# Optimization experiments

Measured on AMD Instinct MI355X. Metric: run time of the kernel, lower is better.

Reference implementation:

```python
import jax, jax.numpy as jnp
import numpy as np

# Mamba2 hyperparameters (from init_kwargs + mamba_ssm defaults)
D_MODEL = 1024
D_STATE = 64
D_CONV = 4
EXPAND = 2
HEADDIM = 64                      # mamba_ssm default
D_INNER = EXPAND * D_MODEL        # 2048
NHEADS = D_INNER // HEADDIM       # 32
NGROUPS = 1
CONV_DIM = D_INNER + 2 * NGROUPS * D_STATE      # 2176
D_IN_PROJ = 2 * D_INNER + 2 * NGROUPS * D_STATE + NHEADS  # 4256
BATCH, SEQLEN = 4, 2048


def setup_inputs() -> dict:
    key = jax.random.key(0)
    ks = jax.random.split(key, 8)
    x = jax.random.normal(ks[0], (BATCH, SEQLEN, D_MODEL), dtype=jnp.float32)
    W_in = jax.random.normal(ks[1], (D_MODEL, D_IN_PROJ), dtype=jnp.float32) * 0.02
    conv_w = jax.random.normal(ks[2], (CONV_DIM, D_CONV), dtype=jnp.float32) * 0.2
    conv_b = jnp.zeros((CONV_DIM,), dtype=jnp.float32)
    # dt_bias = inverse-softplus of dt ~ U(1e-3, 0.1), as in mamba_ssm init
    dt = jnp.exp(jax.random.uniform(ks[3], (NHEADS,)) * (np.log(0.1) - np.log(1e-3)) + np.log(1e-3))
    dt_bias = dt + jnp.log(-jnp.expm1(-dt))
    A_log = jnp.log(jax.random.uniform(ks[4], (NHEADS,), minval=1.0, maxval=16.0))
    D = jnp.ones((NHEADS,), dtype=jnp.float32)
    norm_w = jnp.ones((D_INNER,), dtype=jnp.float32)
    W_out = jax.random.normal(ks[5], (D_INNER, D_MODEL), dtype=jnp.float32) * 0.02
    return {"x": x, "W_in": W_in, "conv_w": conv_w, "conv_b": conv_b,
            "dt_bias": dt_bias, "A_log": A_log, "D": D, "norm_w": norm_w, "W_out": W_out}


def _mamba2_forward(x, W_in, conv_w, conv_b, dt_bias, A_log, D, norm_w, W_out):
    Bsz, L, _ = x.shape
    zxbcdt = x @ W_in                                   # [B, L, D_IN_PROJ]
    z = zxbcdt[..., :D_INNER]                           # gate
    xBC = zxbcdt[..., D_INNER:D_INNER + CONV_DIM]
    dt = zxbcdt[..., D_INNER + CONV_DIM:]               # [B, L, H]
    dt = jax.nn.softplus(dt + dt_bias)

    # causal depthwise conv1d over time, kernel width D_CONV
    xp = jnp.pad(xBC, ((0, 0), (D_CONV - 1, 0), (0, 0)))
    xc = sum(xp[:, k:k + L, :] * conv_w[:, k] for k in range(D_CONV))
    xBC = jax.nn.silu(xc + conv_b)

    xh = xBC[..., :D_INNER].reshape(Bsz, L, NHEADS, HEADDIM)   # [B,L,H,P]
    Bm = xBC[..., D_INNER:D_INNER + D_STATE]                   # [B,L,N] (ngroups=1)
    Cm = xBC[..., D_INNER + D_STATE:]                          # [B,L,N]
    A = -jnp.exp(A_log)                                        # [H]

    # selective SSM scan: h_t = h_{t-1}*exp(dt_t*A) + dt_t * x_t (outer) B_t ; y_t = C_t . h_t
    def step(h, inp):
        dt_t, x_t, B_t, C_t = inp                 # [B,H],[B,H,P],[B,N],[B,N]
        dA = jnp.exp(dt_t * A)                    # [B,H]
        h = h * dA[..., None, None] + (dt_t[..., None] * x_t)[..., None] * B_t[:, None, None, :]
        y_t = jnp.einsum('bhpn,bn->bhp', h, C_t)
        return h, y_t

    h0 = jnp.zeros((Bsz, NHEADS, HEADDIM, D_STATE), dtype=x.dtype)
    inputs = (jnp.moveaxis(dt, 1, 0), jnp.moveaxis(xh, 1, 0),
              jnp.moveaxis(Bm, 1, 0), jnp.moveaxis(Cm, 1, 0))
    _, ys = jax.lax.scan(step, h0, inputs)                     # [L,B,H,P]
    y = jnp.moveaxis(ys, 0, 1) + xh * D[None, None, :, None]   # skip term D*x
    y = y.reshape(Bsz, L, D_INNER)

    # gated RMSNorm: norm(y * silu(z)) * weight
    y = y * jax.nn.silu(z)
    y = y * jax.lax.rsqrt(jnp.mean(y * y, axis=-1, keepdims=True) + 1e-5) * norm_w
    return y @ W_out


def reference(x, W_in, conv_w, conv_b, dt_bias, A_log, D, norm_w, W_out):
    return _mamba2_forward(x, W_in, conv_w, conv_b, dt_bias, A_log, D, norm_w, W_out)
```

## Files before the change

### kernel.cpp

```cpp
#include <hip/hip_runtime.h>
#include <hip/hip_bf16.h>

#define B_SZ   4
#define SEQ    2048
#define DM     1024
#define DIN    2048
#define DST    64
#define NH     32
#define HD     64
#define CONVD  2176
#define DPROJ  4256
#define NPROJ  4224
#define MROWS  (B_SZ*SEQ)
#define QC     64
#define NC     (SEQ/QC)


typedef __attribute__((ext_vector_type(8))) __bf16 bf16x8;
typedef __attribute__((ext_vector_type(4))) __bf16 bf16x4;
typedef __attribute__((ext_vector_type(4))) float  floatx4;

__device__ __forceinline__ int swz(int row, int col) {
    return row * 64 + ((((col >> 3) ^ (row & 7)) << 3) | (col & 7));
}
__device__ __forceinline__ float bfbits2f(unsigned short u) {
    return __uint_as_float(((unsigned int)u) << 16);
}
__device__ __forceinline__ unsigned short f2bfbits(float f) {
    union { __bf16 h; unsigned short u; } cv; cv.h = (__bf16)f; return cv.u;
}

__global__ __launch_bounds__(256) void prep_weights_kernel(const float* __restrict__ W_in,
                                                           const float* __restrict__ W_out,
                                                           const float* __restrict__ norm_w,
                                                           float* __restrict__ dtWc,
                                                           __bf16* __restrict__ WinT,
                                                           __bf16* __restrict__ WoutT) {
    __shared__ float tile[32][129];
    const int bid = blockIdx.x, tid = threadIdx.x;
    if (bid < 128) {
        int idx = bid * 256 + tid;
        int k = idx >> 5, h = idx & 31;
        dtWc[idx] = W_in[(size_t)k * DPROJ + 2 * DIN + 2 * DST + h];
        return;
    }
    const float* src; __bf16* dst; const float* scal; int Ksrc, Csrc, mb, kb;
    if (bid < 128 + 1056) {
        int t = bid - 128; mb = t >> 5; kb = t & 31;
        src = W_in; dst = WinT; scal = nullptr; Ksrc = DM; Csrc = DPROJ;
    } else {
        int t = bid - 1184; mb = t >> 6; kb = t & 63;
        src = W_out; dst = WoutT; scal = norm_w; Ksrc = DIN; Csrc = DM;
    }
    const int K32 = Ksrc >> 5;
    #pragma unroll
    for (int i = 0; i < 4; i++) {
        int idx = tid + 256 * i;
        int kl = idx >> 5, c4 = idx & 31;
        int n = mb * 128 + c4 * 4;
        float4 v = make_float4(0.f, 0.f, 0.f, 0.f);
        if (n < Csrc) v = *(const float4*)(src + (size_t)(kb * 32 + kl) * Csrc + n);
        if (scal) { float s = scal[kb * 32 + kl]; v.x *= s; v.y *= s; v.z *= s; v.w *= s; }
        tile[kl][c4 * 4 + 0] = v.x; tile[kl][c4 * 4 + 1] = v.y;
        tile[kl][c4 * 4 + 2] = v.z; tile[kl][c4 * 4 + 3] = v.w;
    }
    __syncthreads();
    #pragma unroll
    for (int i = 0; i < 2; i++) {
        int c = tid + 256 * i;
        int sub = c >> 6, ln = c & 63, q = ln >> 4, lmn = ln & 15;
        bf16x8 o;
        #pragma unroll
        for (int e = 0; e < 8; e++) o[e] = (__bf16)tile[q * 8 + e][sub * 16 + lmn];
        *(bf16x8*)(dst + ((((size_t)(mb * 8 + sub)) * K32 + kb) << 9) + (ln << 3)) = o;
    }
}

__global__ __launch_bounds__(256) void cvt_dt_kernel(const float* __restrict__ x,
                                                     const float* __restrict__ dtWc,
                                                     __bf16* __restrict__ xbf,
                                                     float* __restrict__ dtraw) {
    __shared__ float xs[16][132];
    __shared__ float dtw[128 * 32];
    const int tid = threadIdx.x;
    const int r0 = blockIdx.x * 16;
    const int lm = tid & 15, pos = tid >> 4;
    const int rr = tid >> 4, h2 = (tid & 15) * 2;
    __bf16* slab = xbf + (size_t)blockIdx.x * (16 * DM);

    float a0 = 0.f, a1 = 0.f;
    for (int kc = 0; kc < 8; kc++) {
        #pragma unroll
        for (int i = 0; i < 2; i++) {
            int idx = tid + 256 * i;
            int row = idx >> 5, c4 = idx & 31;
            float4 v = ((const float4*)(x + (size_t)(r0 + row) * DM + kc * 128))[c4];
            xs[row][c4 * 4 + 0] = v.x; xs[row][c4 * 4 + 1] = v.y;
            xs[row][c4 * 4 + 2] = v.z; xs[row][c4 * 4 + 3] = v.w;
        }
        #pragma unroll
        for (int i = 0; i < 16; i++)
            dtw[tid + 256 * i] = dtWc[kc * 4096 + tid + 256 * i];
        __syncthreads();
        {
            bf16x8 o;
            #pragma unroll
            for (int e = 0; e < 8; e++) o[e] = (__bf16)xs[lm][pos * 8 + e];
            int kb = kc * 4 + (pos >> 2), q = pos & 3;
            *(bf16x8*)(slab + (size_t)(kb * 64 + q * 16 + lm) * 8) = o;
        }
        for (int j = 0; j < 128; j++) {
            float xv = xs[rr][j];
            a0 = fmaf(xv, dtw[j * 32 + h2], a0);
            a1 = fmaf(xv, dtw[j * 32 + h2 + 1], a1);
        }
        __syncthreads();
    }
    dtraw[(size_t)(r0 + rr) * NH + h2]     = a0;
    dtraw[(size_t)(r0 + rr) * NH + h2 + 1] = a1;
}

template<int STORE_BF16>
__global__ __launch_bounds__(256) void gemm_tt_kernel(const __bf16* __restrict__ A,
                                                      const __bf16* __restrict__ Bt,
                                                      float* __restrict__ Cf,
                                                      __bf16* __restrict__ Cb,
                                                      const float* __restrict__ rowscale,
                                                      int N, int K) {
    __shared__ __align__(16) __bf16 As[4096];
    __shared__ __align__(16) __bf16 Bs[4096];
    const int tid = threadIdx.x;
    const int wave = tid >> 6, lane = tid & 63;
    const int lm = lane & 15, lq = lane >> 4;
    const int mb = blockIdx.x, nb = blockIdx.y;
    const int K32 = K >> 5;

    floatx4 acc[4][4] = {};

    for (int kb = 0; kb < K32; kb++) {
        #pragma unroll
        for (int r = 0; r < 2; r++) {
            int c = tid + (r << 8);
            int sub = c >> 6, ln = c & 63;
            __builtin_amdgcn_global_load_lds(
                reinterpret_cast<const unsigned int*>(
                    A + ((((size_t)(mb * 8 + sub)) * K32 + kb) << 9) + (ln << 3)),
                reinterpret_cast<unsigned int*>(As + (size_t)c * 8), 16, 0, 0);
            __builtin_amdgcn_global_load_lds(
                reinterpret_cast<const unsigned int*>(
                    Bt + ((((size_t)(nb * 8 + sub)) * K32 + kb) << 9) + (ln << 3)),
                reinterpret_cast<unsigned int*>(Bs + (size_t)c * 8), 16, 0, 0);
        }
        __syncthreads();
        bf16x8 af[4], bfr[4];
        #pragma unroll
        for (int i = 0; i < 4; i++)
            af[i] = *(const bf16x8*)(As + ((((wave & 1) << 2) + i) << 9) + (lane << 3));
        #pragma unroll
        for (int i = 0; i < 4; i++)
            bfr[i] = *(const bf16x8*)(Bs + ((((wave >> 1) << 2) + i) << 9) + (lane << 3));
        #pragma unroll
        for (int mi = 0; mi < 4; mi++)
            #pragma unroll
            for (int ni = 0; ni < 4; ni++)
                acc[mi][ni] = __builtin_amdgcn_mfma_f32_16x16x32_bf16(af[mi], bfr[ni], acc[mi][ni], 0, 0, 0);
        __syncthreads();
    }

    const int wm = (wave & 1) << 6, wn = (wave >> 1) << 6;
    #pragma unroll
    for (int mi = 0; mi < 4; mi++) {
        #pragma unroll
        for (int r = 0; r < 4; r++) {
            int row = mb * 128 + wm + mi * 16 + lq * 4 + r;
            float s = 1.f;
            if (rowscale) s = rsqrtf(rowscale[row] * (1.f / (float)DIN) + 1e-5f);
            #pragma unroll
            for (int ni = 0; ni < 4; ni++) {
                int col = nb * 128 + wn + ni * 16 + lm;
                if (col < N) {
                    if (STORE_BF16) Cb[(size_t)row * N + col] = (__bf16)acc[mi][ni][r];
                    else            Cf[(size_t)row * N + col] = acc[mi][ni][r] * s;
                }
            }
        }
    }
}

__global__ __launch_bounds__(256) void conv_dt_kernel(const __bf16* __restrict__ zx,
                                                      const float* __restrict__ cw,
                                                      const float* __restrict__ cb,
                                                      __bf16* __restrict__ out,
                                                      const float* __restrict__ dtraw,
                                                      const float* __restrict__ dt_bias,
                                                      const float* __restrict__ A_log,
                                                      float* __restrict__ dtv,
                                                      float* __restrict__ cum,
                                                      float* __restrict__ rowsum) {
    const int bid = blockIdx.x, tid = threadIdx.x;
    if (bid < 1088) {
        const int by = bid / 17, bx = bid - by * 17;
        const int tc = tid & 15, tt = tid >> 4;
        const int c0 = (bx * 16 + tc) * 8;
        const int tg = by * 16 + tt;
        const int b = tg >> 8, t0 = (tg & 255) << 3;

        float xb[11][8];
        #pragma unroll
        for (int i = 0; i < 11; i++) {
            int t = t0 + i - 3;
            if (t >= 0) {
                bf16x8 v = *(const bf16x8*)(zx + ((size_t)(b * SEQ + t)) * NPROJ + DIN + c0);
                #pragma unroll
                for (int j = 0; j < 8; j++) xb[i][j] = (float)v[j];
            } else {
                #pragma unroll
                for (int j = 0; j < 8; j++) xb[i][j] = 0.f;
            }
        }
        float w0[8], w1[8], w2[8], w3[8], bias[8];
        #pragma unroll
        for (int j = 0; j < 8; j++) {
            float4 w = *(const float4*)(cw + (size_t)(c0 + j) * 4);
            w0[j] = w.x; w1[j] = w.y; w2[j] = w.z; w3[j] = w.w;
            bias[j] = cb[c0 + j];
        }
        #pragma unroll
        for (int s = 0; s < 8; s++) {
            bf16x8 o;
            #pragma unroll
            for (int j = 0; j < 8; j++) {
                float v = bias[j] + w0[j] * xb[s][j] + w1[j] * xb[s + 1][j]
                                  + w2[j] * xb[s + 2][j] + w3[j] * xb[s + 3][j];
                o[j] = (__bf16)(v / (1.f + __expf(-v)));
            }
            *(bf16x8*)(out + ((size_t)(b * SEQ + t0 + s)) * CONVD + c0) = o;
        }
    } else if (bid < 1216) {
        const int blk = bid - 1088;
        const int b = blk >> 5, h = blk & 31;
        const int wave = tid >> 6, lane = tid & 63;
        float Ah = -__expf(A_log[h]);
        float dtb = dt_bias[h];
        for (int c = wave; c < NC; c += 4) {
            int t = c * QC + lane;
            float u = dtraw[((size_t)b * SEQ + t) * NH + h] + dtb;
            float d = fmaxf(u, 0.f) + log1pf(__expf(-fabsf(u)));
            float s = d * Ah;
            #pragma unroll
            for (int o = 1; o < 64; o <<= 1) {
                float v = __shfl_up(s, o);
                if (lane >= o) s += v;
            }
            size_t idx = (size_t)blk * SEQ + t;
            dtv[idx] = d;
            cum[idx] = s;
        }
    } else {
        float4 z = make_float4(0.f, 0.f, 0.f, 0.f);
        *(float4*)(rowsum + (size_t)(bid - 1216) * 1024 + tid * 4) = z;
    }
}

__global__ __launch_bounds__(256) void chunk_state_kernel(const __bf16* __restrict__ xc,
                                                          const float* __restrict__ dtv,
                                                          const float* __restrict__ cum,
                                                          __bf16* __restrict__ Sbuf) {
    const int blk = blockIdx.x;
    const int hq = blk & 7;
    const int bc = blk >> 3;
    const int c = bc & (NC - 1), b = bc >> 5;
    const int tid = threadIdx.x;
    const int wave = tid >> 6, lane = tid & 63;
    const int lm = lane & 15, q = lane >> 4;
    const int h = hq * 4 + wave;

    __shared__ __align__(16) __bf16 sBt[4096];
    __shared__ __align__(16) __bf16 sXw[4][4096];

    const size_t rowbase = (size_t)b * SEQ + (size_t)c * QC;
    {
        int k = tid & 31, n0 = (tid >> 5) * 8;
        unsigned short u0[8], u1[8];
        *(uint4*)u0 = *(const uint4*)(xc + (rowbase + 2 * k) * CONVD + DIN + n0);
        *(uint4*)u1 = *(const uint4*)(xc + (rowbase + 2 * k + 1) * CONVD + DIN + n0);
        #pragma unroll
        for (int i = 0; i < 8; i++) {
            unsigned int v = (unsigned int)u0[i] | ((unsigned int)u1[i] << 16);
            ((unsigned int*)sBt)[swz(n0 + i, 2 * k) >> 1] = v;
        }
    }
    const float* cump = cum + (size_t)(b * NH + h) * SEQ + (size_t)c * QC;
    const float* dtp  = dtv + (size_t)(b * NH + h) * SEQ + (size_t)c * QC;
    {
        int k = lane & 31, ph = (lane >> 5) * 32;
        float clast = cump[63];
        float w0 = dtp[2 * k]     * __expf(clast - cump[2 * k]);
        float w1 = dtp[2 * k + 1] * __expf(clast - cump[2 * k + 1]);
        unsigned short u0[32], u1[32];
        const __bf16* r0 = xc + (rowbase + 2 * k) * CONVD + h * 64 + ph;
        const __bf16* r1 = xc + (rowbase + 2 * k + 1) * CONVD + h * 64 + ph;
        #pragma unroll
        for (int i = 0; i < 4; i++) {
            ((uint4*)u0)[i] = ((const uint4*)r0)[i];
            ((uint4*)u1)[i] = ((const uint4*)r1)[i];
        }
        unsigned int* dstw = (unsigned int*)sXw[wave];
        #pragma unroll
        for (int i = 0; i < 32; i++) {
            unsigned int lo = f2bfbits(bfbits2f(u0[i]) * w0);
            unsigned int hi = f2bfbits(bfbits2f(u1[i]) * w1);
            dstw[swz(ph + i, 2 * k) >> 1] = lo | (hi << 16);
        }
    }
    __syncthreads();

    floatx4 acc[4][4] = {};
    #pragma unroll
    for (int kb = 0; kb < 2; kb++) {
        bf16x8 aX[4], bB[4];
        #pragma unroll
        for (int pi = 0; pi < 4; pi++)
            aX[pi] = *(const bf16x8*)(&sXw[wave][swz(pi * 16 + lm, kb * 32 + q * 8)]);
        #pragma unroll
        for (int ni = 0; ni < 4; ni++)
            bB[ni] = *(const bf16x8*)(&sBt[swz(ni * 16 + lm, kb * 32 + q * 8)]);
        #pragma unroll
        for (int pi = 0; pi < 4; pi++)
            #pragma unroll
            for (int ni = 0; ni < 4; ni++)
                acc[pi][ni] = __builtin_amdgcn_mfma_f32_16x16x32_bf16(aX[pi], bB[ni], acc[pi][ni], 0, 0, 0);
    }
    __bf16* Sp = Sbuf + ((size_t)(b * NC + c) * NH + h) * (HD * DST);
    #pragma unroll
    for (int pi = 0; pi < 4; pi++)
        #pragma unroll
        for (int r = 0; r < 4; r++) {
            int p = pi * 16 + q * 4 + r;
            #pragma unroll
            for (int ni = 0; ni < 4; ni++)
                Sp[p * 64 + ni * 16 + lm] = (__bf16)acc[pi][ni][r];
        }
}

__global__ __launch_bounds__(256) void state_scan_kernel(__bf16* __restrict__ Sbuf,
                                                         const float* __restrict__ cum) {
    int blk = blockIdx.x >> 2;
    int part = blockIdx.x & 3;
    int b = blk >> 5, h = blk & 31;
    int off = part * 1024 + threadIdx.x * 4;
    float run[4];
    #pragma unroll
    for (int n = 0; n < 4; n++) run[n] = 0.f;
    for (int c = 0; c < NC; c++) {
        __bf16* Sp = Sbuf + ((size_t)(b * NC + c) * NH + h) * (HD * DST) + off;
        bf16x4 sv = *(const bf16x4*)Sp;
        float tmp[4];
        #pragma unroll
        for (int n = 0; n < 4; n++) tmp[n] = (float)sv[n];
        bf16x4 ov;
        #pragma unroll
        for (int n = 0; n < 4; n++) ov[n] = (__bf16)run[n];
        *(bf16x4*)Sp = ov;
        float P = __expf(cum[(size_t)blk * SEQ + c * QC + QC - 1]);
        #pragma unroll
        for (int n = 0; n < 4; n++) run[n] = fmaf(run[n], P, tmp[n]);
    }
}

__global__ __launch_bounds__(128) void chunk_out_kernel(const __bf16* __restrict__ xc,
                                                        const float* __restrict__ dtv,
                                                        const float* __restrict__ cum,
                                                        const __bf16* __restrict__ Sbuf,
                                                        const float* __restrict__ Dv,
                                                        const __bf16* __restrict__ zx,
                                                        float* __restrict__ rowsum,
                                                        __bf16* __restrict__ y) {
    const int blk = blockIdx.x;
    const int hp = blk & 15;
    const int bc = blk >> 4;
    const int c = bc & (NC - 1), b = bc >> 5;
    const int tid = threadIdx.x;
    const int wave = tid >> 6, lane = tid & 63;
    const int lm = lane & 15, q = lane >> 4;
    const int h = hp * 2 + wave;

    __shared__ __align__(16) __bf16 smem[16384];
    __bf16* sB  = smem;
    __bf16* sC  = smem + 4096;
    __bf16* sXt = smem + 8192 + (wave << 12);
    __bf16* sP  = smem + (wave << 12);

    const size_t rowbase = (size_t)b * SEQ + (size_t)c * QC;
    {
        int r = tid >> 1, c0 = (tid & 1) * 32;
        const __bf16* gB = xc + (rowbase + r) * CONVD + DIN + c0;
        const __bf16* gC = xc + (rowbase + r) * CONVD + DIN + DST + c0;
        #pragma unroll
        for (int i = 0; i < 4; i++) {
            *(uint4*)(&sB[swz(r, c0 + i * 8)]) = *(const uint4*)(gB + i * 8);
            *(uint4*)(&sC[swz(r, c0 + i * 8)]) = *(const uint4*)(gC + i * 8);
        }
    }
    {
        int k = lane & 31, ph = (lane >> 5) * 32;
        unsigned short u0[32], u1[32];
        const __bf16* r0 = xc + (rowbase + 2 * k) * CONVD + h * 64 + ph;
        const __bf16* r1 = xc + (rowbase + 2 * k + 1) * CONVD + h * 64 + ph;
        #pragma unroll
        for (int i = 0; i < 4; i++) {
            ((uint4*)u0)[i] = ((const uint4*)r0)[i];
            ((uint4*)u1)[i] = ((const uint4*)r1)[i];
        }
        unsigned int* dstw = (unsigned int*)sXt;
        #pragma unroll
        for (int i = 0; i < 32; i++)
            dstw[swz(ph + i, 2 * k) >> 1] = (unsigned int)u0[i] | ((unsigned int)u1[i] << 16);
    }
    __syncthreads();

    const float* cump = cum + (size_t)(b * NH + h) * SEQ + (size_t)c * QC;
    const float* dtp  = dtv + (size_t)(b * NH + h) * SEQ + (size_t)c * QC;
    float cumv = cump[lane], dtvv = dtp[lane];
    float ct[4][4];
    #pragma unroll
    for (int ti = 0; ti < 4; ti++)
        #pragma unroll
        for (int r = 0; r < 4; r++)
            ct[ti][r] = __shfl(cumv, ti * 16 + q * 4 + r);
    float cums_l[4], dtv_l[4];
    #pragma unroll
    for (int si = 0; si < 4; si++) {
        cums_l[si] = __shfl(cumv, si * 16 + lm);
        dtv_l[si]  = __shfl(dtvv, si * 16 + lm);
    }

    bf16x8 afC[4][2];
    #pragma unroll
    for (int ti = 0; ti < 4; ti++)
        #pragma unroll
        for (int kb = 0; kb < 2; kb++)
            afC[ti][kb] = *(const bf16x8*)(&sC[swz(ti * 16 + lm, kb * 32 + q * 8)]);

    floatx4 accG[4][4] = {};
    #pragma unroll
    for (int kb = 0; kb < 2; kb++) {
        bf16x8 bfB[4];
        #pragma unroll
        for (int si = 0; si < 4; si++)
            bfB[si] = *(const bf16x8*)(&sB[swz(si * 16 + lm, kb * 32 + q * 8)]);
        #pragma unroll
        for (int ti = 0; ti < 4; ti++)
            #pragma unroll
            for (int si = 0; si < 4; si++)
                if (si <= ti)
                    accG[ti][si] = __builtin_amdgcn_mfma_f32_16x16x32_bf16(afC[ti][kb], bfB[si], accG[ti][si], 0, 0, 0);
    }
    __syncthreads();

    float Dh = Dv[h];
    #pragma unroll
    for (int ti = 0; ti < 4; ti++)
        #pragma unroll
        for (int si = 0; si < 4; si++) {
            if (si > ti) continue;
            #pragma unroll
            for (int r = 0; r < 4; r++) {
                int t = ti * 16 + q * 4 + r;
                float arg = fminf(ct[ti][r] - cums_l[si], 0.f);
                float val = dtv_l[si] * __expf(arg) * accG[ti][si][r];
                if (ti == si) {
                    if (lm > q * 4 + r) val = 0.f;
                    else if (lm == q * 4 + r) val += Dh;
                }
                sP[swz(t, si * 16 + lm)] = (__bf16)val;
            }
        }
    #pragma unroll
    for (int r = 0; r < 4; r++) {
        sP[swz(q * 4 + r, 16 + lm)] = (__bf16)0.f;
        sP[swz(32 + q * 4 + r, 48 + lm)] = (__bf16)0.f;
    }
    __syncthreads();

    floatx4 accY[4][4] = {};
    const __bf16* Sp = Sbuf + ((size_t)(b * NC + c) * NH + h) * (HD * DST);
    #pragma unroll
    for (int kb = 0; kb < 2; kb++) {
        bf16x8 bS[4];
        #pragma unroll
        for (int pi = 0; pi < 4; pi++)
            bS[pi] = *(const bf16x8*)(Sp + (pi * 16 + lm) * 64 + kb * 32 + q * 8);
        #pragma unroll
        for (int ti = 0; ti < 4; ti++)
            #pragma unroll
            for (int pi = 0; pi < 4; pi++)
                accY[ti][pi] = __builtin_amdgcn_mfma_f32_16x16x32_bf16(afC[ti][kb], bS[pi], accY[ti][pi], 0, 0, 0);
    }
    #pragma unroll
    for (int ti = 0; ti < 4; ti++)
        #pragma unroll
        for (int r = 0; r < 4; r++) {
            float e = __expf(ct[ti][r]);
            #pragma unroll
            for (int pi = 0; pi < 4; pi++)
                accY[ti][pi][r] *= e;
        }

    #pragma unroll
    for (int kb = 0; kb < 2; kb++) {
        bf16x8 bX[4];
        #pragma unroll
        for (int pi = 0; pi < 4; pi++)
            bX[pi] = *(const bf16x8*)(&sXt[swz(pi * 16 + lm, kb * 32 + q * 8)]);
        #pragma unroll
        for (int ti = 0; ti < 4; ti++) {
            if (ti < 2 * kb) continue;
            bf16x8 aP = *(const bf16x8*)(&sP[swz(ti * 16 + lm, kb * 32 + q * 8)]);
            #pragma unroll
            for (int pi = 0; pi < 4; pi++)
                accY[ti][pi] = __builtin_amdgcn_mfma_f32_16x16x32_bf16(aP, bX[pi], accY[ti][pi], 0, 0, 0);
        }
    }

    const int R4v = (int)(rowbase >> 4);
    #pragma unroll
    for (int ti = 0; ti < 4; ti++) {
        __bf16* slab = y + (size_t)(R4v + ti) * 32768;
        #pragma unroll
        for (int r = 0; r < 4; r++) {
            int t = ti * 16 + q * 4 + r;
            const __bf16* zrow = zx + (rowbase + t) * NPROJ + h * 64;
            float rs = 0.f;
            #pragma unroll
            for (int pi = 0; pi < 4; pi++) {
                float zv = (float)zrow[pi * 16 + lm];
                float g = accY[ti][pi][r] * (zv / (1.f + __expf(-zv)));
                rs += g * g;
                int kbC = h * 2 + (pi >> 1);
                int qC  = ((pi & 1) << 1) + (lm >> 3);
                slab[kbC * 512 + qC * 128 + (lm & 7) + (q * 4 + r) * 8] = (__bf16)g;
            }
            rs += __shfl_xor(rs, 1);
            rs += __shfl_xor(rs, 2);
            rs += __shfl_xor(rs, 4);
            rs += __shfl_xor(rs, 8);
            if (lm == 0) atomicAdd(&rowsum[rowbase + t], rs);
        }
    }
}

extern "C" void kernel_launch(void* const* d_in, const int* in_sizes, int n_in,
                              void* d_out, int out_size, void* d_ws, size_t ws_size,
                              hipStream_t stream) {
    const float* x       = (const float*)d_in[0];
    const float* W_in    = (const float*)d_in[1];
    const float* conv_w  = (const float*)d_in[2];
    const float* conv_b  = (const float*)d_in[3];
    const float* dt_bias = (const float*)d_in[4];
    const float* A_log   = (const float*)d_in[5];
    const float* Dv      = (const float*)d_in[6];
    const float* norm_w  = (const float*)d_in[7];
    const float* W_out   = (const float*)d_in[8];
    float* out = (float*)d_out;

    char* ws = (char*)d_ws;
    size_t off = 0;
    auto take = [&](size_t bytes) { void* p = ws + off; off = (off + bytes + 255) & ~(size_t)255; return p; };
    __bf16* xbf    = (__bf16*)take((size_t)MROWS * DM * 2);
    __bf16* WinT   = (__bf16*)take((size_t)NPROJ * DM * 2);
    __bf16* WoutT  = (__bf16*)take((size_t)DM * DIN * 2);
    __bf16* zx     = (__bf16*)take((size_t)MROWS * NPROJ * 2);
    __bf16* xc     = (__bf16*)take((size_t)MROWS * CONVD * 2);
    __bf16* yf     = (__bf16*)take((size_t)MROWS * DIN * 2);
    float*  dtraw  = (float*) take((size_t)MROWS * NH * 4);
    float*  dtv    = (float*) take((size_t)B_SZ * NH * SEQ * 4);
    float*  cum    = (float*) take((size_t)B_SZ * NH * SEQ * 4);
    __bf16* Sbuf   = (__bf16*)take((size_t)B_SZ * NC * NH * HD * DST * 2);
    float*  dtWc   = (float*) take((size_t)DM * NH * 4);
    float*  rowsum = (float*) take((size_t)MROWS * 4);
    (void)ws_size;

    prep_weights_kernel<<<dim3(1696), 256, 0, stream>>>(W_in, W_out, norm_w, dtWc, WinT, WoutT);
    cvt_dt_kernel<<<dim3(MROWS / 16), 256, 0, stream>>>(x, dtWc, xbf, dtraw);
    gemm_tt_kernel<1><<<dim3(MROWS / 128, NPROJ / 128), 256, 0, stream>>>(
        xbf, WinT, nullptr, zx, nullptr, NPROJ, DM);
    conv_dt_kernel<<<dim3(1224), 256, 0, stream>>>(zx, conv_w, conv_b, xc,
                                                   dtraw, dt_bias, A_log, dtv, cum, rowsum);
    chunk_state_kernel<<<dim3(B_SZ * NC * (NH / 4)), 256, 0, stream>>>(xc, dtv, cum, Sbuf);
    state_scan_kernel<<<dim3(B_SZ * NH * 4), 256, 0, stream>>>(Sbuf, cum);
    chunk_out_kernel<<<dim3(B_SZ * NC * (NH / 2)), 128, 0, stream>>>(
        xc, dtv, cum, Sbuf, Dv, zx, rowsum, yf);
    gemm_tt_kernel<0><<<dim3(MROWS / 128, DM / 128), 256, 0, stream>>>(
        yf, WoutT, out, nullptr, rowsum, DM, DIN);
}
```

Measured before the change: 379.6 us.

## Fold dt/cumsum work into in-proj GEMM launch and shrink cvt_dt tiles

The dt softplus/cumsum blocks and the rowsum zeroing move out of the conv kernel and are appended as extra blocks to the first GEMM launch, so they run alongside GEMM tiles. The causal conv becomes its own kernel with a 2D grid. cvt_dt now processes 4 rows per block, splitting the dt projection across 8 partial sums with a shared reduction, which raises block count and drops the large shared dtw staging. Risks include GEMM tail imbalance from the mixed block types and more launches of cvt_dt.

```diff
diff --git a/kernel.cpp b/kernel.cpp
--- a/kernel.cpp
+++ b/kernel.cpp
@@ -26,9 +26,7 @@
 __device__ __forceinline__ float bfbits2f(unsigned short u) {
     return __uint_as_float(((unsigned int)u) << 16);
 }
-__device__ __forceinline__ unsigned short f2bfbits(float f) {
-    union { __bf16 h; unsigned short u; } cv; cv.h = (__bf16)f; return cv.u;
-}
+__device__ __forceinline__ float silu_f(float v) { return v / (1.f + __expf(-v)); }
 
 __global__ __launch_bounds__(256) void prep_weights_kernel(const float* __restrict__ W_in,
                                                            const float* __restrict__ W_out,
@@ -41,7 +39,7 @@
     if (bid < 128) {
         int idx = bid * 256 + tid;
         int k = idx >> 5, h = idx & 31;
-        dtWc[idx] = W_in[(size_t)k * DPROJ + 2 * DIN + 2 * DST + h];
+        dtWc[idx] = W_in[(size_t)k * DPROJ + NPROJ + h];
         return;
     }
     const float* src; __bf16* dst; const float* scal; int Ksrc, Csrc, mb, kb;
@@ -80,59 +78,64 @@
                                                      const float* __restrict__ dtWc,
                                                      __bf16* __restrict__ xbf,
                                                      float* __restrict__ dtraw) {
-    __shared__ float xs[16][132];
-    __shared__ float dtw[128 * 32];
+    __shared__ float xs[4][DM];
+    __shared__ float red[4][8][32];
+    const int row0 = blockIdx.x * 4;
     const int tid = threadIdx.x;
-    const int r0 = blockIdx.x * 16;
-    const int lm = tid & 15, pos = tid >> 4;
-    const int rr = tid >> 4, h2 = (tid & 15) * 2;
-    __bf16* slab = xbf + (size_t)blockIdx.x * (16 * DM);
-
-    float a0 = 0.f, a1 = 0.f;
-    for (int kc = 0; kc < 8; kc++) {
-        #pragma unroll
-        for (int i = 0; i < 2; i++) {
-            int idx = tid + 256 * i;
-            int row = idx >> 5, c4 = idx & 31;
-            float4 v = ((const float4*)(x + (size_t)(r0 + row) * DM + kc * 128))[c4];
-            xs[row][c4 * 4 + 0] = v.x; xs[row][c4 * 4 + 1] = v.y;
-            xs[row][c4 * 4 + 2] = v.z; xs[row][c4 * 4 + 3] = v.w;
-        }
-        #pragma unroll
-        for (int i = 0; i < 16; i++)
-            dtw[tid + 256 * i] = dtWc[kc * 4096 + tid + 256 * i];
-        __syncthreads();
-        {
-            bf16x8 o;
-            #pragma unroll
-            for (int e = 0; e < 8; e++) o[e] = (__bf16)xs[lm][pos * 8 + e];
-            int kb = kc * 4 + (pos >> 2), q = pos & 3;
-            *(bf16x8*)(slab + (size_t)(kb * 64 + q * 16 + lm) * 8) = o;
-        }
-        for (int j = 0; j < 128; j++) {
-            float xv = xs[rr][j];
-            a0 = fmaf(xv, dtw[j * 32 + h2], a0);
-            a1 = fmaf(xv, dtw[j * 32 + h2 + 1], a1);
-        }
-        __syncthreads();
-    }
-    dtraw[(size_t)(r0 + rr) * NH + h2]     = a0;
-    dtraw[(size_t)(r0 + rr) * NH + h2 + 1] = a1;
+    #pragma unroll
+    for (int r = 0; r < 4; r++) {
+        float4 v = ((const float4*)(x + (size_t)(row0 + r) * DM))[tid];
+        xs[r][tid * 4 + 0] = v.x; xs[r][tid * 4 + 1] = v.y;
+        xs[r][tid * 4 + 2] = v.z; xs[r][tid * 4 + 3] = v.w;
+    }
+    __syncthreads();
+    __bf16* slab = xbf + (size_t)(row0 >> 4) * (16 * DM);
+    const int lmb = row0 & 15;
+    #pragma unroll
+    for (int i = 0; i < 2; i++) {
+        int g = tid + 256 * i;
+        int r = g >> 7, pos = g & 127;
+        int kb = pos >> 2, q = pos & 3;
+        bf16x8 o;
+        #pragma unroll
+        for (int e = 0; e < 8; e++) o[e] = (__bf16)xs[r][pos * 8 + e];
+        *(bf16x8*)(slab + (size_t)(kb * 64 + q * 16 + lmb + r) * 8) = o;
+    }
+    const int part = tid >> 5, h = tid & 31;
+    const float* wb = dtWc + part * 128 * 32 + h;
+    const int kb0 = part * 128;
+    float s0 = 0.f, s1 = 0.f, s2 = 0.f, s3 = 0.f;
+    for (int j = 0; j < 128; j++) {
+        float w = wb[j * 32];
+        s0 = fmaf(xs[0][kb0 + j], w, s0);
+        s1 = fmaf(xs[1][kb0 + j], w, s1);
+        s2 = fmaf(xs[2][kb0 + j], w, s2);
+        s3 = fmaf(xs[3][kb0 + j], w, s3);
+    }
+    red[0][part][h] = s0; red[1][part][h] = s1;
+    red[2][part][h] = s2; red[3][part][h] = s3;
+    __syncthreads();
+    if (tid < 128) {
+        int r = tid >> 5, hh = tid & 31;
+        float s = 0.f;
+        #pragma unroll
+        for (int p = 0; p < 8; p++) s += red[r][p][hh];
+        dtraw[(size_t)(row0 + r) * NH + hh] = s;
+    }
 }
 
 template<int STORE_BF16>
-__global__ __launch_bounds__(256) void gemm_tt_kernel(const __bf16* __restrict__ A,
-                                                      const __bf16* __restrict__ Bt,
-                                                      float* __restrict__ Cf,
-                                                      __bf16* __restrict__ Cb,
-                                                      const float* __restrict__ rowscale,
-                                                      int N, int K) {
+__device__ __forceinline__ void gemm_body(const __bf16* __restrict__ A,
+                                          const __bf16* __restrict__ Bt,
+                                          float* __restrict__ Cf,
+                                          __bf16* __restrict__ Cb,
+                                          const float* __restrict__ rowscale,
+                                          int N, int K, int mb, int nb) {
     __shared__ __align__(16) __bf16 As[4096];
     __shared__ __align__(16) __bf16 Bs[4096];
     const int tid = threadIdx.x;
     const int wave = tid >> 6, lane = tid & 63;
     const int lm = lane & 15, lq = lane >> 4;
-    const int mb = blockIdx.x, nb = blockIdx.y;
     const int K32 = K >> 5;
 
     floatx4 acc[4][4] = {};
@@ -187,57 +190,20 @@
     }
 }
 
-__global__ __launch_bounds__(256) void conv_dt_kernel(const __bf16* __restrict__ zx,
-                                                      const float* __restrict__ cw,
-                                                      const float* __restrict__ cb,
-                                                      __bf16* __restrict__ out,
-                                                      const float* __restrict__ dtraw,
-                                                      const float* __restrict__ dt_bias,
-                                                      const float* __restrict__ A_log,
-                                                      float* __restrict__ dtv,
-                                                      float* __restrict__ cum,
-                                                      float* __restrict__ rowsum) {
+__global__ __launch_bounds__(256) void gemm1_kernel(const __bf16* __restrict__ A,
+                                                    const __bf16* __restrict__ Bt,
+                                                    __bf16* __restrict__ Cb,
+                                                    const float* __restrict__ dtraw,
+                                                    const float* __restrict__ dt_bias,
+                                                    const float* __restrict__ A_log,
+                                                    float* __restrict__ dtv,
+                                                    float* __restrict__ cum,
+                                                    float* __restrict__ rowsum) {
     const int bid = blockIdx.x, tid = threadIdx.x;
-    if (bid < 1088) {
-        const int by = bid / 17, bx = bid - by * 17;
-        const int tc = tid & 15, tt = tid >> 4;
-        const int c0 = (bx * 16 + tc) * 8;
-        const int tg = by * 16 + tt;
-        const int b = tg >> 8, t0 = (tg & 255) << 3;
-
-        float xb[11][8];
-        #pragma unroll
-        for (int i = 0; i < 11; i++) {
-            int t = t0 + i - 3;
-            if (t >= 0) {
-                bf16x8 v = *(const bf16x8*)(zx + ((size_t)(b * SEQ + t)) * NPROJ + DIN + c0);
-                #pragma unroll
-                for (int j = 0; j < 8; j++) xb[i][j] = (float)v[j];
-            } else {
-                #pragma unroll
-                for (int j = 0; j < 8; j++) xb[i][j] = 0.f;
-            }
-        }
-        float w0[8], w1[8], w2[8], w3[8], bias[8];
-        #pragma unroll
-        for (int j = 0; j < 8; j++) {
-            float4 w = *(const float4*)(cw + (size_t)(c0 + j) * 4);
-            w0[j] = w.x; w1[j] = w.y; w2[j] = w.z; w3[j] = w.w;
-            bias[j] = cb[c0 + j];
-        }
-        #pragma unroll
-        for (int s = 0; s < 8; s++) {
-            bf16x8 o;
-            #pragma unroll
-            for (int j = 0; j < 8; j++) {
-                float v = bias[j] + w0[j] * xb[s][j] + w1[j] * xb[s + 1][j]
-                                  + w2[j] * xb[s + 2][j] + w3[j] * xb[s + 3][j];
-                o[j] = (__bf16)(v / (1.f + __expf(-v)));
-            }
-            *(bf16x8*)(out + ((size_t)(b * SEQ + t0 + s)) * CONVD + c0) = o;
-        }
-    } else if (bid < 1216) {
-        const int blk = bid - 1088;
+    if (bid < 2112) {
+        gemm_body<1>(A, Bt, nullptr, Cb, nullptr, NPROJ, DM, bid & 63, bid >> 6);
+    } else if (bid < 2240) {
+        const int blk = bid - 2112;
         const int b = blk >> 5, h = blk & 31;
         const int wave = tid >> 6, lane = tid & 63;
         float Ah = -__expf(A_log[h]);
@@ -258,7 +224,57 @@
         }
     } else {
         float4 z = make_float4(0.f, 0.f, 0.f, 0.f);
-        *(float4*)(rowsum + (size_t)(bid - 1216) * 1024 + tid * 4) = z;
+        *(float4*)(rowsum + (size_t)(bid - 2240) * 1024 + tid * 4) = z;
+    }
+}
+
+__global__ __launch_bounds__(256) void gemm2_kernel(const __bf16* __restrict__ A,
+                                                    const __bf16* __restrict__ Bt,
+                                                    float* __restrict__ Cf,
+                                                    const float* __restrict__ rowscale) {
+    gemm_body<0>(A, Bt, Cf, nullptr, rowscale, DM, DIN, blockIdx.x, blockIdx.y);
+}
+
+__global__ __launch_bounds__(256) void conv_silu_kernel(const __bf16* __restrict__ zx,
+                                                        const float* __restrict__ cw,
+                                                        const float* __restrict__ cb,
+                                                        __bf16* __restrict__ out) {
+    const int tid = threadIdx.x;
+    const int tc = tid & 15, tt = tid >> 4;
+    const int c0 = (blockIdx.x * 16 + tc) * 8;
+    const int tg = blockIdx.y * 16 + tt;
+    const int b = tg >> 8, t0 = (tg & 255) << 3;
+
+    float xb[11][8];
+    #pragma unroll
+    for (int i = 0; i < 11; i++) {
+        int t = t0 + i - 3;
+        if (t >= 0) {
+            bf16x8 v = *(const bf16x8*)(zx + ((size_t)(b * SEQ + t)) * NPROJ + DIN + c0);
+            #pragma unroll
+            for (int j = 0; j < 8; j++) xb[i][j] = (float)v[j];
+        } else {
+            #pragma unroll
+            for (int j = 0; j < 8; j++) xb[i][j] = 0.f;
+        }
+    }
+    float w0[8], w1[8], w2[8], w3[8], bias[8];
+    #pragma unroll
+    for (int j = 0; j < 8; j++) {
+        float4 w = *(const float4*)(cw + (size_t)(c0 + j) * 4);
+        w0[j] = w.x; w1[j] = w.y; w2[j] = w.z; w3[j] = w.w;
+        bias[j] = cb[c0 + j];
+    }
+    #pragma unroll
+    for (int s = 0; s < 8; s++) {
+        bf16x8 o;
+        #pragma unroll
+        for (int j = 0; j < 8; j++) {
+            float v = bias[j] + w0[j] * xb[s][j] + w1[j] * xb[s + 1][j]
+                              + w2[j] * xb[s + 2][j] + w3[j] * xb[s + 3][j];
+            o[j] = (__bf16)silu_f(v);
+        }
+        *(bf16x8*)(out + ((size_t)(b * SEQ + t0 + s)) * CONVD + c0) = o;
     }
 }
 
@@ -308,9 +324,10 @@
         unsigned int* dstw = (unsigned int*)sXw[wave];
         #pragma unroll
         for (int i = 0; i < 32; i++) {
-            unsigned int lo = f2bfbits(bfbits2f(u0[i]) * w0);
-            unsigned int hi = f2bfbits(bfbits2f(u1[i]) * w1);
-            dstw[swz(ph + i, 2 * k) >> 1] = lo | (hi << 16);
+            union { __bf16 hh; unsigned short us; } lo, hi;
+            lo.hh = (__bf16)(bfbits2f(u0[i]) * w0);
+            hi.hh = (__bf16)(bfbits2f(u1[i]) * w1);
+            dstw[swz(ph + i, 2 * k) >> 1] = (unsigned int)lo.us | ((unsigned int)hi.us << 16);
         }
     }
     __syncthreads();
@@ -535,7 +552,7 @@
             #pragma unroll
             for (int pi = 0; pi < 4; pi++) {
                 float zv = (float)zrow[pi * 16 + lm];
-                float g = accY[ti][pi][r] * (zv / (1.f + __expf(-zv)));
+                float g = accY[ti][pi][r] * silu_f(zv);
                 rs += g * g;
                 int kbC = h * 2 + (pi >> 1);
                 int qC  = ((pi & 1) << 1) + (lm >> 3);
@@ -582,15 +599,13 @@
     (void)ws_size;
 
     prep_weights_kernel<<<dim3(1696), 256, 0, stream>>>(W_in, W_out, norm_w, dtWc, WinT, WoutT);
-    cvt_dt_kernel<<<dim3(MROWS / 16), 256, 0, stream>>>(x, dtWc, xbf, dtraw);
-    gemm_tt_kernel<1><<<dim3(MROWS / 128, NPROJ / 128), 256, 0, stream>>>(
-        xbf, WinT, nullptr, zx, nullptr, NPROJ, DM);
-    conv_dt_kernel<<<dim3(1224), 256, 0, stream>>>(zx, conv_w, conv_b, xc,
-                                                   dtraw, dt_bias, A_log, dtv, cum, rowsum);
+    cvt_dt_kernel<<<dim3(MROWS / 4), 256, 0, stream>>>(x, dtWc, xbf, dtraw);
+    gemm1_kernel<<<dim3(2248), 256, 0, stream>>>(xbf, WinT, zx,
+                                                 dtraw, dt_bias, A_log, dtv, cum, rowsum);
+    conv_silu_kernel<<<dim3(17, 64), 256, 0, stream>>>(zx, conv_w, conv_b, xc);
     chunk_state_kernel<<<dim3(B_SZ * NC * (NH / 4)), 256, 0, stream>>>(xc, dtv, cum, Sbuf);
     state_scan_kernel<<<dim3(B_SZ * NH * 4), 256, 0, stream>>>(Sbuf, cum);
     chunk_out_kernel<<<dim3(B_SZ * NC * (NH / 2)), 128, 0, stream>>>(
         xc, dtv, cum, Sbuf, Dv, zx, rowsum, yf);
-    gemm_tt_kernel<0><<<dim3(MROWS / 128, DM / 128), 256, 0, stream>>>(
-        yf, WoutT, out, nullptr, rowsum, DM, DIN);
-}
+    gemm2_kernel<<<dim3(MROWS / 128, DM / 128), 256, 0, stream>>>(yf, WoutT, out, rowsum);
+}
```

Measured after the change: 351.6 us. -7.4%, faster.
